# Kernel optimization log

Hardware: AMD Instinct MI355X
Metric: run time of the kernel (lower is better)

The kernel has to match this reference:

```python
import jax, jax.numpy as jnp
import numpy as np
import math

D_MODEL = 2048
N_HEADS = 16
BATCH = 2
SEQ = 2048
ALIBI_BIAS_MAX = 8


def alibi_bias(n_heads, seq_len, alibi_bias_max=8):
    # matches torch alibi_bias(full=False): shape [1, n_heads, 1, seq_len]
    dist = jnp.arange(1 - seq_len, 1, dtype=jnp.float32).reshape(1, 1, 1, seq_len)
    m = jnp.arange(1, n_heads + 1, dtype=jnp.float32) * (alibi_bias_max / n_heads)
    slopes = 1.0 / (2.0 ** m).reshape(1, n_heads, 1, 1)
    return dist * slopes


def setup_inputs() -> dict:
    key = jax.random.key(0)
    ks = jax.random.split(key, 5)
    d = D_MODEL
    scale = 1.0 / math.sqrt(d)
    x = jax.random.normal(ks[0], (BATCH, SEQ, d), dtype=jnp.float32)
    w_qkv = jax.random.normal(ks[1], (3 * d, d), dtype=jnp.float32) * scale
    b_qkv = jnp.zeros((3 * d,), dtype=jnp.float32)
    w_out = jax.random.normal(ks[2], (d, d), dtype=jnp.float32) * scale
    b_out = jnp.zeros((d,), dtype=jnp.float32)
    attn_mask = alibi_bias(N_HEADS, SEQ, ALIBI_BIAS_MAX)
    return {"x": x, "attn_mask": attn_mask, "w_qkv": w_qkv, "b_qkv": b_qkv,
            "w_out": w_out, "b_out": b_out}


def reference(x, attn_mask, w_qkv, b_qkv, w_out, b_out):
    B, S, D = x.shape
    H = N_HEADS
    hd = D // H
    # packed QKV projection
    qkv = x @ w_qkv.T + b_qkv                      # [B,S,3D]
    qkv = qkv.reshape(B, S, 3, H, hd)
    q, k, v = qkv[:, :, 0], qkv[:, :, 1], qkv[:, :, 2]  # [B,S,H,hd]
    scores = jnp.einsum('bqhd,bkhd->bhqk', q, k) * (1.0 / math.sqrt(hd))
    scores = scores + attn_mask                    # ALiBi additive bias [1,H,1,S]
    causal = jnp.tril(jnp.ones((S, S), dtype=bool))
    scores = jnp.where(causal, scores, -jnp.inf)
    probs = jax.nn.softmax(scores, axis=-1)        # [B,H,S,S]
    ctx = jnp.einsum('bhqk,bkhd->bqhd', probs, v).reshape(B, S, D)
    return ctx @ w_out.T + b_out
```

## Files before the change

### kernel.cpp

```cpp
#include <hip/hip_runtime.h>
#include <math.h>

typedef unsigned short u16;
typedef __attribute__((ext_vector_type(8))) short short8;
typedef __attribute__((ext_vector_type(4))) float f32x4;

#define MFMA16x16x32(a, b, c) __builtin_amdgcn_mfma_f32_16x16x32_bf16((a), (b), (c), 0, 0, 0)

__device__ __forceinline__ u16 f32_to_bf16(float x) {
  union { float f; unsigned u; } v; v.f = x;
  unsigned r = v.u + 0x7FFFu + ((v.u >> 16) & 1u);
  return (u16)(r >> 16);
}

__global__ void cvt_f32_bf16(const float* __restrict__ in, u16* __restrict__ out, int n4) {
  int i = blockIdx.x * blockDim.x + threadIdx.x;
  int stride = gridDim.x * blockDim.x;
  for (; i < n4; i += stride) {
    float4 v = ((const float4*)in)[i];
    ushort4 o;
    o.x = f32_to_bf16(v.x);
    o.y = f32_to_bf16(v.y);
    o.z = f32_to_bf16(v.z);
    o.w = f32_to_bf16(v.w);
    ((ushort4*)out)[i] = o;
  }
}

template <int OUT_BF16>
__global__ __launch_bounds__(256) void gemm_nt(
    const u16* __restrict__ A,
    const u16* __restrict__ B,
    const float* __restrict__ bias,
    void* __restrict__ C,
    int M, int N, int K)
{
  __shared__ u16 As[128 * 32];
  __shared__ u16 Bs[128 * 32];
  const int tid = threadIdx.x;
  const int w = tid >> 6, l = tid & 63;
  const int l15 = l & 15, l4 = l >> 4;
  const int wm = w >> 1, wn = w & 1;
  const long bm = (long)blockIdx.y * 128, bn = (long)blockIdx.x * 128;

  const f32x4 z4 = {0.f, 0.f, 0.f, 0.f};
  f32x4 acc[4][4];
  #pragma unroll
  for (int m = 0; m < 4; ++m)
    #pragma unroll
    for (int n = 0; n < 4; ++n) acc[m][n] = z4;

  const int srow = l >> 2;
  const int scol = (l & 3) * 8;

  const int nkt = K >> 5;
  for (int kt = 0; kt < nkt; ++kt) {
    const int k0 = kt << 5;
    #pragma unroll
    for (int j = 0; j < 2; ++j) {
      const int rbase = w * 32 + j * 16;
      const u16* ga = A + (bm + rbase + srow) * (long)K + k0 + scol;
      __builtin_amdgcn_global_load_lds(
          (const __attribute__((address_space(1))) void*)ga,
          (__attribute__((address_space(3))) void*)(As + rbase * 32), 16, 0, 0);
      const u16* gb = B + (bn + rbase + srow) * (long)K + k0 + scol;
      __builtin_amdgcn_global_load_lds(
          (const __attribute__((address_space(1))) void*)gb,
          (__attribute__((address_space(3))) void*)(Bs + rbase * 32), 16, 0, 0);
    }
    __syncthreads();
    short8 af[4], bf[4];
    #pragma unroll
    for (int m = 0; m < 4; ++m)
      af[m] = *(const short8*)(As + (wm * 64 + m * 16 + l15) * 32 + l4 * 8);
    #pragma unroll
    for (int n = 0; n < 4; ++n)
      bf[n] = *(const short8*)(Bs + (wn * 64 + n * 16 + l15) * 32 + l4 * 8);
    #pragma unroll
    for (int m = 0; m < 4; ++m)
      #pragma unroll
      for (int n = 0; n < 4; ++n)
        acc[m][n] = MFMA16x16x32(af[m], bf[n], acc[m][n]);
    __syncthreads();
  }

  #pragma unroll
  for (int m = 0; m < 4; ++m) {
    const long row0 = bm + wm * 64 + m * 16 + l4 * 4;
    #pragma unroll
    for (int n = 0; n < 4; ++n) {
      const long col = bn + wn * 64 + n * 16 + l15;
      const float bv = bias[col];
      #pragma unroll
      for (int r = 0; r < 4; ++r) {
        const float v = acc[m][n][r] + bv;
        if (OUT_BF16)
          ((u16*)C)[(row0 + r) * (long)N + col] = f32_to_bf16(v);
        else
          ((float*)C)[(row0 + r) * (long)N + col] = v;
      }
    }
  }
}

__global__ __launch_bounds__(256) void repack_kv(
    const u16* __restrict__ qkv, u16* __restrict__ kimg, u16* __restrict__ vimg)
{
  const int t = blockIdx.x;
  const int h = blockIdx.y, b = blockIdx.z;
  const int tid = threadIdx.x;
  __shared__ u16 Vl[64][136];

  const long qbase = ((long)(b * 2048 + t * 64)) * 6144 + h * 128;
  u16* kout = kimg + (((long)(b * 16 + h) * 32 + t) * 8192);
  u16* vout = vimg + (((long)(b * 16 + h) * 32 + t) * 8192);

  #pragma unroll
  for (int i = 0; i < 4; ++i) {
    const int j = tid + i * 256;
    {
      const int r = j >> 4, c8 = (j & 15) * 8;
      uint4 v = *(const uint4*)(qkv + qbase + (long)r * 6144 + 4096 + c8);
      *(uint4*)(&Vl[r][c8]) = v;
    }
    {
      const int byte = j * 16;
      const int r = byte >> 8;
      const int wv = (byte & 255) ^ ((r & 7) << 4);
      const int d0 = wv >> 1;
      uint4 v = *(const uint4*)(qkv + qbase + (long)r * 6144 + 2048 + d0);
      *(uint4*)(kout + j * 8) = v;
    }
  }
  __syncthreads();
  #pragma unroll
  for (int i = 0; i < 4; ++i) {
    const int j = tid + i * 256;
    const int byte = j * 16;
    const int d = byte >> 7;
    const int wv = (byte & 127) ^ ((d & 7) << 4);
    const int k0 = wv >> 1;
    u16 tmp[8];
    #pragma unroll
    for (int m = 0; m < 8; ++m) tmp[m] = Vl[k0 + m][d];
    *(uint4*)(vout + j * 8) = *(const uint4*)tmp;
  }
}

__global__ __launch_bounds__(256) void attn_kernel(
    const u16* __restrict__ qkv,
    const u16* __restrict__ kimg,
    const u16* __restrict__ vimg,
    u16* __restrict__ ctx)
{
  const int S = 2048, NHD = 6144, NT = 32;
  const int p = blockIdx.x, h = blockIdx.y, b = blockIdx.z;
  const int tid = threadIdx.x;
  const int w = tid >> 6, l = tid & 63;
  const int l15 = l & 15, l4 = l >> 4;

  __shared__ u16 Ks[64 * 128];
  __shared__ u16 Vt[128 * 64];
  __shared__ u16 Ps[4][16 * 64];

  const float LOG2E = 1.44269504088896f;
  const float c1 = 0.08838834764831845f * LOG2E;
  const float slope2 = exp2f(-0.5f * (float)(h + 1)) * LOG2E;

  const f32x4 z4 = {0.f, 0.f, 0.f, 0.f};

  for (int pass = 0; pass < 2; ++pass) {
    const int qblk = pass ? (NT - 1 - p) : p;
    const int qb0 = qblk * 64;

    short8 qf[4];
    {
      const int qrow = qb0 + w * 16 + l15;
      const u16* qp = qkv + (long)(b * S + qrow) * NHD + h * 128 + l4 * 8;
      #pragma unroll
      for (int kc = 0; kc < 4; ++kc) qf[kc] = *(const short8*)(qp + kc * 32);
    }

    f32x4 o[8];
    #pragma unroll
    for (int i = 0; i < 8; ++i) o[i] = z4;
    float m_r[4] = {-3.0e38f, -3.0e38f, -3.0e38f, -3.0e38f};
    float l_r[4] = {0.f, 0.f, 0.f, 0.f};

    for (int kt = 0; kt <= qblk; ++kt) {
      const u16* ksrc = kimg + (((long)(b * 16 + h) * NT + kt) * 8192);
      const u16* vsrc = vimg + (((long)(b * 16 + h) * NT + kt) * 8192);
      #pragma unroll
      for (int i = 0; i < 4; ++i) {
        const int chunk = w * 4 + i;
        __builtin_amdgcn_global_load_lds(
            (const __attribute__((address_space(1))) void*)(ksrc + chunk * 512 + l * 8),
            (__attribute__((address_space(3))) void*)(Ks + chunk * 512), 16, 0, 0);
        __builtin_amdgcn_global_load_lds(
            (const __attribute__((address_space(1))) void*)(vsrc + chunk * 512 + l * 8),
            (__attribute__((address_space(3))) void*)(Vt + chunk * 512), 16, 0, 0);
      }
      __syncthreads();

      f32x4 sf[4];
      #pragma unroll
      for (int nt = 0; nt < 4; ++nt) sf[nt] = z4;
      #pragma unroll
      for (int nt = 0; nt < 4; ++nt) {
        const int krow = nt * 16 + l15;
        #pragma unroll
        for (int kc = 0; kc < 4; ++kc) {
          int kbyte = (krow * 256 + kc * 64 + l4 * 16) ^ ((krow & 7) << 4);
          const short8 kf = *(const short8*)((const char*)Ks + kbyte);
          sf[nt] = MFMA16x16x32(qf[kc], kf, sf[nt]);
        }
      }

      float add_nt[4];
      int kg_nt[4];
      #pragma unroll
      for (int nt = 0; nt < 4; ++nt) {
        kg_nt[nt] = kt * 64 + nt * 16 + l15;
        add_nt[nt] = slope2 * (float)(kg_nt[nt] - (S - 1));
      }
      const bool diag = (kt == qblk);
      float alpha[4];
      #pragma unroll
      for (int r = 0; r < 4; ++r) {
        const int qrow_l = l4 * 4 + r;
        const int qg = qb0 + w * 16 + qrow_l;
        float sc[4];
        #pragma unroll
        for (int nt = 0; nt < 4; ++nt) sc[nt] = sf[nt][r] * c1 + add_nt[nt];
        if (diag) {
          #pragma unroll
          for (int nt = 0; nt < 4; ++nt)
            if (kg_nt[nt] > qg) sc[nt] = -3.0e38f;
        }
        float mx = fmaxf(fmaxf(sc[0], sc[1]), fmaxf(sc[2], sc[3]));
        #pragma unroll
        for (int d = 1; d < 16; d <<= 1) mx = fmaxf(mx, __shfl_xor(mx, d, 64));
        const float mnew = fmaxf(m_r[r], mx);
        float sum = 0.f;
        #pragma unroll
        for (int nt = 0; nt < 4; ++nt) {
          const float pv = exp2f(sc[nt] - mnew);
          sc[nt] = pv;
          sum += pv;
        }
        #pragma unroll
        for (int d = 1; d < 16; d <<= 1) sum += __shfl_xor(sum, d, 64);
        alpha[r] = exp2f(m_r[r] - mnew);
        l_r[r] = l_r[r] * alpha[r] + sum;
        m_r[r] = mnew;
        #pragma unroll
        for (int nt = 0; nt < 4; ++nt) {
          int pbyte = ((qrow_l * 64 + nt * 16 + l15) * 2) ^ ((qrow_l & 7) << 4);
          *(u16*)((char*)&Ps[w][0] + pbyte) = f32_to_bf16(sc[nt]);
        }
      }

      #pragma unroll
      for (int nt = 0; nt < 8; ++nt)
        #pragma unroll
        for (int r = 0; r < 4; ++r) o[nt][r] *= alpha[r];

      #pragma unroll
      for (int kc = 0; kc < 2; ++kc) {
        int pbyte = ((l15 * 64 + kc * 32 + l4 * 8) * 2) ^ ((l15 & 7) << 4);
        const short8 pf = *(const short8*)((const char*)&Ps[w][0] + pbyte);
        #pragma unroll
        for (int nt = 0; nt < 8; ++nt) {
          const int d = nt * 16 + l15;
          const int vbyte = ((d * 128 + kc * 64 + l4 * 16)) ^ ((d & 7) << 4);
          const short8 vf = *(const short8*)((const char*)Vt + vbyte);
          o[nt] = MFMA16x16x32(pf, vf, o[nt]);
        }
      }
      __syncthreads();
    }

    float rl[4];
    #pragma unroll
    for (int r = 0; r < 4; ++r) rl[r] = 1.0f / l_r[r];
    #pragma unroll
    for (int nt = 0; nt < 8; ++nt) {
      #pragma unroll
      for (int r = 0; r < 4; ++r) {
        const int qg = qb0 + w * 16 + l4 * 4 + r;
        ctx[(long)(b * S + qg) * 2048 + h * 128 + nt * 16 + l15] =
            f32_to_bf16(o[nt][r] * rl[r]);
      }
    }
  }
}

extern "C" void kernel_launch(void* const* d_in, const int* in_sizes, int n_in,
                              void* d_out, int out_size, void* d_ws, size_t ws_size,
                              hipStream_t stream) {
  const float* x     = (const float*)d_in[0];
  const float* w_qkv = (const float*)d_in[2];
  const float* b_qkv = (const float*)d_in[3];
  const float* w_out = (const float*)d_in[4];
  const float* b_out = (const float*)d_in[5];
  float* out = (float*)d_out;

  char* ws = (char*)d_ws;
  u16* xb    = (u16*)(ws);
  u16* wqkvb = (u16*)(ws + 16777216UL);
  u16* woutb = (u16*)(ws + 41943040UL);
  u16* qkvb  = (u16*)(ws + 50331648UL);
  u16* ctxb  = (u16*)(ws + 100663296UL);
  u16* kimg  = (u16*)(ws);
  u16* vimg  = (u16*)(ws + 16777216UL);

  cvt_f32_bf16<<<2048, 256, 0, stream>>>(x, xb, 8388608 / 4);
  cvt_f32_bf16<<<2048, 256, 0, stream>>>(w_qkv, wqkvb, 12582912 / 4);
  cvt_f32_bf16<<<2048, 256, 0, stream>>>(w_out, woutb, 4194304 / 4);

  gemm_nt<1><<<dim3(48, 32), 256, 0, stream>>>(xb, wqkvb, b_qkv, (void*)qkvb, 4096, 6144, 2048);

  repack_kv<<<dim3(32, 16, 2), 256, 0, stream>>>(qkvb, kimg, vimg);

  attn_kernel<<<dim3(16, 16, 2), 256, 0, stream>>>(qkvb, kimg, vimg, ctxb);

  gemm_nt<0><<<dim3(16, 32), 256, 0, stream>>>(ctxb, woutb, b_out, (void*)out, 4096, 2048, 2048);
}
```

Before: 352.0 us.

## Rewrite projection GEMMs with 8-wave 128x256 tiles, double-buffered swizzled LDS

Replaces the 4-wave 128x128 GEMM with an 8-wave 128x256 kernel that stages 64-wide K slices into double-buffered LDS using an XOR swizzle. The next tile's loads are issued before computing the current one, with explicit vmcnt waits. The B half-tile load is split so it overlaps the first half of the MFMA work, and s_setprio raises priority around the MFMA blocks. The aim is to hide global-load latency, avoid LDS bank conflicts and halve the barrier count per K element, at the cost of 96KB of LDS per block and hand-tuned waitcnt logic.

```diff
diff --git a/kernel.cpp b/kernel.cpp
--- a/kernel.cpp
+++ b/kernel.cpp
@@ -6,6 +6,10 @@
 typedef __attribute__((ext_vector_type(4))) float f32x4;
 
 #define MFMA16x16x32(a, b, c) __builtin_amdgcn_mfma_f32_16x16x32_bf16((a), (b), (c), 0, 0, 0)
+#define GLL16(g, s)                                                        \
+  __builtin_amdgcn_global_load_lds(                                        \
+      (const __attribute__((address_space(1))) void*)(g),                  \
+      (__attribute__((address_space(3))) void*)(s), 16, 0, 0)
 
 __device__ __forceinline__ u16 f32_to_bf16(float x) {
   union { float f; unsigned u; } v; v.f = x;
@@ -28,20 +32,36 @@
 }
 
 template <int OUT_BF16>
-__global__ __launch_bounds__(256) void gemm_nt(
+__global__ __launch_bounds__(512, 2) void gemm_nt_8p(
     const u16* __restrict__ A,
     const u16* __restrict__ B,
     const float* __restrict__ bias,
     void* __restrict__ C,
     int M, int N, int K)
 {
-  __shared__ u16 As[128 * 32];
-  __shared__ u16 Bs[128 * 32];
+  __shared__ u16 As[2][8192];
+  __shared__ u16 Bs[2][16384];
+
   const int tid = threadIdx.x;
   const int w = tid >> 6, l = tid & 63;
   const int l15 = l & 15, l4 = l >> 4;
-  const int wm = w >> 1, wn = w & 1;
-  const long bm = (long)blockIdx.y * 128, bn = (long)blockIdx.x * 128;
+  const int wm = w >> 2, wn = w & 3;
+  const long bm = (long)blockIdx.y * 128, bn = (long)blockIdx.x * 256;
+  const int NT = K >> 6;
+
+  const u16 *aSrc0, *aSrc1, *bSrc0, *bSrc1;
+  {
+    int q = w * 2048 + l * 16;
+    int r = q >> 7, cb = (q & 127) ^ ((r & 7) << 4);
+    aSrc0 = A + (bm + r) * (long)K + (cb >> 1);
+    bSrc0 = B + (bn + r) * (long)K + (cb >> 1);
+    q += 1024;
+    r = q >> 7; cb = (q & 127) ^ ((r & 7) << 4);
+    aSrc1 = A + (bm + r) * (long)K + (cb >> 1);
+    bSrc1 = B + (bn + r) * (long)K + (cb >> 1);
+  }
+  const long bHS = 128 * (long)K;
+  const int ldsA = w * 1024;
 
   const f32x4 z4 = {0.f, 0.f, 0.f, 0.f};
   f32x4 acc[4][4];
@@ -50,38 +70,81 @@
     #pragma unroll
     for (int n = 0; n < 4; ++n) acc[m][n] = z4;
 
-  const int srow = l >> 2;
-  const int scol = (l & 3) * 8;
-
-  const int nkt = K >> 5;
-  for (int kt = 0; kt < nkt; ++kt) {
-    const int k0 = kt << 5;
-    #pragma unroll
-    for (int j = 0; j < 2; ++j) {
-      const int rbase = w * 32 + j * 16;
-      const u16* ga = A + (bm + rbase + srow) * (long)K + k0 + scol;
-      __builtin_amdgcn_global_load_lds(
-          (const __attribute__((address_space(1))) void*)ga,
-          (__attribute__((address_space(3))) void*)(As + rbase * 32), 16, 0, 0);
-      const u16* gb = B + (bn + rbase + srow) * (long)K + k0 + scol;
-      __builtin_amdgcn_global_load_lds(
-          (const __attribute__((address_space(1))) void*)gb,
-          (__attribute__((address_space(3))) void*)(Bs + rbase * 32), 16, 0, 0);
-    }
-    __syncthreads();
-    short8 af[4], bf[4];
+  const int xo0 = (l4 * 16) ^ ((l15 & 7) << 4);
+  const int xo1 = (64 + l4 * 16) ^ ((l15 & 7) << 4);
+  const char* aRd = (const char*)&As[0][0] + (wm * 64 + l15) * 128;
+  const char* bRd = (const char*)&Bs[0][0] + (wn * 32 + l15) * 128;
+
+  GLL16(aSrc0, &As[0][ldsA]);
+  GLL16(aSrc1, &As[0][ldsA + 512]);
+  GLL16(bSrc0, &Bs[0][ldsA]);
+  GLL16(bSrc1, &Bs[0][ldsA + 512]);
+  GLL16(bSrc0 + bHS, &Bs[0][8192 + ldsA]);
+  GLL16(bSrc1 + bHS, &Bs[0][8192 + ldsA + 512]);
+
+  short8 af[4][2], bf[4][2];
+
+  for (int t = 0; t < NT; ++t) {
+    const int nxt = t + 1;
+    const int bufo = t & 1;
+
+    if (nxt < NT) {
+      const long ko = (long)nxt * 64;
+      const int nb = nxt & 1;
+      GLL16(aSrc0 + ko, &As[nb][ldsA]);
+      GLL16(aSrc1 + ko, &As[nb][ldsA + 512]);
+      GLL16(bSrc0 + ko, &Bs[nb][ldsA]);
+      GLL16(bSrc1 + ko, &Bs[nb][ldsA + 512]);
+      asm volatile("s_waitcnt vmcnt(6)\ns_barrier" ::: "memory");
+    } else {
+      asm volatile("s_waitcnt vmcnt(2)\ns_barrier" ::: "memory");
+    }
+    const char* ab = aRd + bufo * 16384;
+    const char* bb = bRd + bufo * 32768;
+    #pragma unroll
+    for (int m = 0; m < 4; ++m) {
+      af[m][0] = *(const short8*)(ab + m * 2048 + xo0);
+      af[m][1] = *(const short8*)(ab + m * 2048 + xo1);
+    }
+    #pragma unroll
+    for (int n = 0; n < 2; ++n) {
+      bf[n][0] = *(const short8*)(bb + n * 2048 + xo0);
+      bf[n][1] = *(const short8*)(bb + n * 2048 + xo1);
+    }
+    __builtin_amdgcn_s_setprio(1);
     #pragma unroll
     for (int m = 0; m < 4; ++m)
-      af[m] = *(const short8*)(As + (wm * 64 + m * 16 + l15) * 32 + l4 * 8);
-    #pragma unroll
-    for (int n = 0; n < 4; ++n)
-      bf[n] = *(const short8*)(Bs + (wn * 64 + n * 16 + l15) * 32 + l4 * 8);
+      #pragma unroll
+      for (int n = 0; n < 2; ++n) {
+        acc[m][n] = MFMA16x16x32(af[m][0], bf[n][0], acc[m][n]);
+        acc[m][n] = MFMA16x16x32(af[m][1], bf[n][1], acc[m][n]);
+      }
+    __builtin_amdgcn_s_setprio(0);
+
+    if (nxt < NT) {
+      const long ko = (long)nxt * 64;
+      const int nb = nxt & 1;
+      GLL16(bSrc0 + bHS + ko, &Bs[nb][8192 + ldsA]);
+      GLL16(bSrc1 + bHS + ko, &Bs[nb][8192 + ldsA + 512]);
+      asm volatile("s_waitcnt vmcnt(6)\ns_barrier" ::: "memory");
+    } else {
+      asm volatile("s_waitcnt vmcnt(0)\ns_barrier" ::: "memory");
+    }
+    const char* bb1 = bb + 16384;
+    #pragma unroll
+    for (int n = 0; n < 2; ++n) {
+      bf[2 + n][0] = *(const short8*)(bb1 + n * 2048 + xo0);
+      bf[2 + n][1] = *(const short8*)(bb1 + n * 2048 + xo1);
+    }
+    __builtin_amdgcn_s_setprio(1);
     #pragma unroll
     for (int m = 0; m < 4; ++m)
       #pragma unroll
-      for (int n = 0; n < 4; ++n)
-        acc[m][n] = MFMA16x16x32(af[m], bf[n], acc[m][n]);
-    __syncthreads();
+      for (int n = 2; n < 4; ++n) {
+        acc[m][n] = MFMA16x16x32(af[m][0], bf[n][0], acc[m][n]);
+        acc[m][n] = MFMA16x16x32(af[m][1], bf[n][1], acc[m][n]);
+      }
+    __builtin_amdgcn_s_setprio(0);
   }
 
   #pragma unroll
@@ -89,7 +152,7 @@
     const long row0 = bm + wm * 64 + m * 16 + l4 * 4;
     #pragma unroll
     for (int n = 0; n < 4; ++n) {
-      const long col = bn + wn * 64 + n * 16 + l15;
+      const long col = bn + wn * 32 + (n & 1) * 16 + (n >> 1) * 128 + l15;
       const float bv = bias[col];
       #pragma unroll
       for (int r = 0; r < 4; ++r) {
@@ -318,11 +381,11 @@
   cvt_f32_bf16<<<2048, 256, 0, stream>>>(w_qkv, wqkvb, 12582912 / 4);
   cvt_f32_bf16<<<2048, 256, 0, stream>>>(w_out, woutb, 4194304 / 4);
 
-  gemm_nt<1><<<dim3(48, 32), 256, 0, stream>>>(xb, wqkvb, b_qkv, (void*)qkvb, 4096, 6144, 2048);
+  gemm_nt_8p<1><<<dim3(24, 32), 512, 0, stream>>>(xb, wqkvb, b_qkv, (void*)qkvb, 4096, 6144, 2048);
 
   repack_kv<<<dim3(32, 16, 2), 256, 0, stream>>>(qkvb, kimg, vimg);
 
   attn_kernel<<<dim3(16, 16, 2), 256, 0, stream>>>(qkvb, kimg, vimg, ctxb);
 
-  gemm_nt<0><<<dim3(16, 32), 256, 0, stream>>>(ctxb, woutb, b_out, (void*)out, 4096, 2048, 2048);
-}
+  gemm_nt_8p<0><<<dim3(8, 32), 512, 0, stream>>>(ctxb, woutb, b_out, (void*)out, 4096, 2048, 2048);
+}
```

Result: faster. 309.9 us, median of 4 (-12.0%).

## Triple-buffer GEMM with swizzled async LDS loads and batch softmax reductions

Applied to the files above, without the earlier changes.

Rewrites the bf16 GEMM main loop as a three-stage ring of LDS buffers. Global-to-LDS loads are issued two K-tiles ahead, the layout is XOR-swizzled to avoid bank conflicts, there is one barrier per iteration, and MFMA priority is raised. It also merges the three f32-to-bf16 conversion launches into one kernel and restructures the attention softmax so the row max and sum shuffles for all four rows are interleaved. The aim is to hide global memory latency behind MFMA work, cut launch overhead and shorten shuffle dependency chains, at the cost of more LDS use (48KB per block) and tighter manual waitcnt reasoning.

```diff
diff --git a/kernel.cpp b/kernel.cpp
--- a/kernel.cpp
+++ b/kernel.cpp
@@ -6,6 +6,10 @@
 typedef __attribute__((ext_vector_type(4))) float f32x4;
 
 #define MFMA16x16x32(a, b, c) __builtin_amdgcn_mfma_f32_16x16x32_bf16((a), (b), (c), 0, 0, 0)
+#define GLL16(g, s)                                                        \
+  __builtin_amdgcn_global_load_lds(                                        \
+      (const __attribute__((address_space(1))) void*)(g),                  \
+      (__attribute__((address_space(3))) void*)(s), 16, 0, 0)
 
 __device__ __forceinline__ u16 f32_to_bf16(float x) {
   union { float f; unsigned u; } v; v.f = x;
@@ -13,35 +17,64 @@
   return (u16)(r >> 16);
 }
 
-__global__ void cvt_f32_bf16(const float* __restrict__ in, u16* __restrict__ out, int n4) {
-  int i = blockIdx.x * blockDim.x + threadIdx.x;
-  int stride = gridDim.x * blockDim.x;
-  for (; i < n4; i += stride) {
-    float4 v = ((const float4*)in)[i];
-    ushort4 o;
-    o.x = f32_to_bf16(v.x);
-    o.y = f32_to_bf16(v.y);
-    o.z = f32_to_bf16(v.z);
-    o.w = f32_to_bf16(v.w);
-    ((ushort4*)out)[i] = o;
-  }
+__device__ __forceinline__ void cvt4(const float* in, u16* out, int j) {
+  float4 v = ((const float4*)in)[j];
+  ushort4 o;
+  o.x = f32_to_bf16(v.x);
+  o.y = f32_to_bf16(v.y);
+  o.z = f32_to_bf16(v.z);
+  o.w = f32_to_bf16(v.w);
+  ((ushort4*)out)[j] = o;
+}
+
+__global__ void cvt_all(const float* __restrict__ x, const float* __restrict__ wq,
+                        const float* __restrict__ wo, u16* __restrict__ xb,
+                        u16* __restrict__ wqb, u16* __restrict__ wob) {
+  const int stride = gridDim.x * blockDim.x;
+  const int i = blockIdx.x * blockDim.x + threadIdx.x;
+  for (int j = i; j < 2097152; j += stride) cvt4(x, xb, j);
+  for (int j = i; j < 3145728; j += stride) cvt4(wq, wqb, j);
+  for (int j = i; j < 1048576; j += stride) cvt4(wo, wob, j);
 }
 
 template <int OUT_BF16>
-__global__ __launch_bounds__(256) void gemm_nt(
+__global__ __launch_bounds__(256, 3) void gemm_k32(
     const u16* __restrict__ A,
     const u16* __restrict__ B,
     const float* __restrict__ bias,
     void* __restrict__ C,
     int M, int N, int K)
 {
-  __shared__ u16 As[128 * 32];
-  __shared__ u16 Bs[128 * 32];
+  __shared__ u16 As[3][4096];
+  __shared__ u16 Bs[3][4096];
+
   const int tid = threadIdx.x;
   const int w = tid >> 6, l = tid & 63;
   const int l15 = l & 15, l4 = l >> 4;
   const int wm = w >> 1, wn = w & 1;
   const long bm = (long)blockIdx.y * 128, bn = (long)blockIdx.x * 128;
+  const int NT = K >> 5;
+
+  const int h = (l & 7) ^ (l >> 3);
+  const int rowoff = 2 * (l >> 3) + (h >> 2);
+  const int colofs = (h & 3) * 8;
+  const int c0 = (w & 1) * 4;
+  const u16* sbase = (w < 2) ? (A + bm * (long)K) : (B + bn * (long)K);
+  const u16* src0 = sbase + (long)(16 * (c0 + 0) + rowoff) * K + colofs;
+  const u16* src1 = sbase + (long)(16 * (c0 + 1) + rowoff) * K + colofs;
+  const u16* src2 = sbase + (long)(16 * (c0 + 2) + rowoff) * K + colofs;
+  const u16* src3 = sbase + (long)(16 * (c0 + 3) + rowoff) * K + colofs;
+
+#define STAGE4(tt)                                                            \
+  do {                                                                        \
+    const int _b = (tt) % 3;                                                  \
+    const long _ko = (long)(tt) * 32;                                         \
+    u16* _d = (w < 2) ? &As[_b][c0 * 512] : &Bs[_b][c0 * 512];                \
+    GLL16(src0 + _ko, _d);                                                    \
+    GLL16(src1 + _ko, _d + 512);                                              \
+    GLL16(src2 + _ko, _d + 1024);                                             \
+    GLL16(src3 + _ko, _d + 1536);                                             \
+  } while (0)
 
   const f32x4 z4 = {0.f, 0.f, 0.f, 0.f};
   f32x4 acc[4][4];
@@ -50,39 +83,40 @@
     #pragma unroll
     for (int n = 0; n < 4; ++n) acc[m][n] = z4;
 
-  const int srow = l >> 2;
-  const int scol = (l & 3) * 8;
-
-  const int nkt = K >> 5;
-  for (int kt = 0; kt < nkt; ++kt) {
-    const int k0 = kt << 5;
-    #pragma unroll
-    for (int j = 0; j < 2; ++j) {
-      const int rbase = w * 32 + j * 16;
-      const u16* ga = A + (bm + rbase + srow) * (long)K + k0 + scol;
-      __builtin_amdgcn_global_load_lds(
-          (const __attribute__((address_space(1))) void*)ga,
-          (__attribute__((address_space(3))) void*)(As + rbase * 32), 16, 0, 0);
-      const u16* gb = B + (bn + rbase + srow) * (long)K + k0 + scol;
-      __builtin_amdgcn_global_load_lds(
-          (const __attribute__((address_space(1))) void*)gb,
-          (__attribute__((address_space(3))) void*)(Bs + rbase * 32), 16, 0, 0);
-    }
-    __syncthreads();
+  const int inner = ((l15 & 1) * 64 + l4 * 16) ^ ((l15 >> 1) << 4);
+  const int rbase = (l15 >> 1) * 128 + inner;
+  const int aOfs = wm * 4096 + rbase;
+  const int bOfs = wn * 4096 + rbase;
+
+  STAGE4(0);
+  STAGE4(1);
+  asm volatile("s_waitcnt vmcnt(4)" ::: "memory");
+  __builtin_amdgcn_s_barrier();
+
+  for (int t = 0; t < NT; ++t) {
+    const char* aT = (const char*)&As[t % 3][0];
+    const char* bT = (const char*)&Bs[t % 3][0];
     short8 af[4], bf[4];
     #pragma unroll
-    for (int m = 0; m < 4; ++m)
-      af[m] = *(const short8*)(As + (wm * 64 + m * 16 + l15) * 32 + l4 * 8);
-    #pragma unroll
-    for (int n = 0; n < 4; ++n)
-      bf[n] = *(const short8*)(Bs + (wn * 64 + n * 16 + l15) * 32 + l4 * 8);
+    for (int m = 0; m < 4; ++m) af[m] = *(const short8*)(aT + aOfs + m * 1024);
+    #pragma unroll
+    for (int n = 0; n < 4; ++n) bf[n] = *(const short8*)(bT + bOfs + n * 1024);
+    if (t + 2 < NT) {
+      STAGE4(t + 2);
+      asm volatile("s_waitcnt vmcnt(4) lgkmcnt(0)" ::: "memory");
+    } else {
+      asm volatile("s_waitcnt vmcnt(0) lgkmcnt(0)" ::: "memory");
+    }
+    __builtin_amdgcn_s_setprio(1);
     #pragma unroll
     for (int m = 0; m < 4; ++m)
       #pragma unroll
       for (int n = 0; n < 4; ++n)
         acc[m][n] = MFMA16x16x32(af[m], bf[n], acc[m][n]);
-    __syncthreads();
-  }
+    __builtin_amdgcn_s_setprio(0);
+    __builtin_amdgcn_s_barrier();
+  }
+#undef STAGE4
 
   #pragma unroll
   for (int m = 0; m < 4; ++m) {
@@ -224,39 +258,53 @@
         add_nt[nt] = slope2 * (float)(kg_nt[nt] - (S - 1));
       }
       const bool diag = (kt == qblk);
-      float alpha[4];
+      float sc[4][4], mxv[4];
+      #pragma unroll
+      for (int r = 0; r < 4; ++r) {
+        const int qg = qb0 + w * 16 + l4 * 4 + r;
+        #pragma unroll
+        for (int nt = 0; nt < 4; ++nt) {
+          float s = sf[nt][r] * c1 + add_nt[nt];
+          if (diag && kg_nt[nt] > qg) s = -3.0e38f;
+          sc[r][nt] = s;
+        }
+        mxv[r] = fmaxf(fmaxf(sc[r][0], sc[r][1]), fmaxf(sc[r][2], sc[r][3]));
+      }
+      #pragma unroll
+      for (int d = 1; d < 16; d <<= 1) {
+        #pragma unroll
+        for (int r = 0; r < 4; ++r)
+          mxv[r] = fmaxf(mxv[r], __shfl_xor(mxv[r], d, 64));
+      }
+      float alpha[4], sum[4];
+      #pragma unroll
+      for (int r = 0; r < 4; ++r) {
+        const float mnew = fmaxf(m_r[r], mxv[r]);
+        sum[r] = 0.f;
+        #pragma unroll
+        for (int nt = 0; nt < 4; ++nt) {
+          const float pv = exp2f(sc[r][nt] - mnew);
+          sc[r][nt] = pv;
+          sum[r] += pv;
+        }
+        alpha[r] = exp2f(m_r[r] - mnew);
+        m_r[r] = mnew;
+      }
+      #pragma unroll
+      for (int d = 1; d < 16; d <<= 1) {
+        #pragma unroll
+        for (int r = 0; r < 4; ++r) sum[r] += __shfl_xor(sum[r], d, 64);
+      }
+      #pragma unroll
+      for (int r = 0; r < 4; ++r) l_r[r] = l_r[r] * alpha[r] + sum[r];
+
       #pragma unroll
       for (int r = 0; r < 4; ++r) {
         const int qrow_l = l4 * 4 + r;
-        const int qg = qb0 + w * 16 + qrow_l;
-        float sc[4];
-        #pragma unroll
-        for (int nt = 0; nt < 4; ++nt) sc[nt] = sf[nt][r] * c1 + add_nt[nt];
-        if (diag) {
-          #pragma unroll
-          for (int nt = 0; nt < 4; ++nt)
-            if (kg_nt[nt] > qg) sc[nt] = -3.0e38f;
-        }
-        float mx = fmaxf(fmaxf(sc[0], sc[1]), fmaxf(sc[2], sc[3]));
-        #pragma unroll
-        for (int d = 1; d < 16; d <<= 1) mx = fmaxf(mx, __shfl_xor(mx, d, 64));
-        const float mnew = fmaxf(m_r[r], mx);
-        float sum = 0.f;
-        #pragma unroll
-        for (int nt = 0; nt < 4; ++nt) {
-          const float pv = exp2f(sc[nt] - mnew);
-          sc[nt] = pv;
-          sum += pv;
-        }
-        #pragma unroll
-        for (int d = 1; d < 16; d <<= 1) sum += __shfl_xor(sum, d, 64);
-        alpha[r] = exp2f(m_r[r] - mnew);
-        l_r[r] = l_r[r] * alpha[r] + sum;
-        m_r[r] = mnew;
         #pragma unroll
         for (int nt = 0; nt < 4; ++nt) {
           int pbyte = ((qrow_l * 64 + nt * 16 + l15) * 2) ^ ((qrow_l & 7) << 4);
-          *(u16*)((char*)&Ps[w][0] + pbyte) = f32_to_bf16(sc[nt]);
+          *(u16*)((char*)&Ps[w][0] + pbyte) = f32_to_bf16(sc[r][nt]);
         }
       }
 
@@ -314,15 +362,13 @@
   u16* kimg  = (u16*)(ws);
   u16* vimg  = (u16*)(ws + 16777216UL);
 
-  cvt_f32_bf16<<<2048, 256, 0, stream>>>(x, xb, 8388608 / 4);
-  cvt_f32_bf16<<<2048, 256, 0, stream>>>(w_qkv, wqkvb, 12582912 / 4);
-  cvt_f32_bf16<<<2048, 256, 0, stream>>>(w_out, woutb, 4194304 / 4);
-
-  gemm_nt<1><<<dim3(48, 32), 256, 0, stream>>>(xb, wqkvb, b_qkv, (void*)qkvb, 4096, 6144, 2048);
+  cvt_all<<<2048, 256, 0, stream>>>(x, w_qkv, w_out, xb, wqkvb, woutb);
+
+  gemm_k32<1><<<dim3(48, 32), 256, 0, stream>>>(xb, wqkvb, b_qkv, (void*)qkvb, 4096, 6144, 2048);
 
   repack_kv<<<dim3(32, 16, 2), 256, 0, stream>>>(qkvb, kimg, vimg);
 
   attn_kernel<<<dim3(16, 16, 2), 256, 0, stream>>>(qkvb, kimg, vimg, ctxb);
 
-  gemm_nt<0><<<dim3(16, 32), 256, 0, stream>>>(ctxb, woutb, b_out, (void*)out, 4096, 2048, 2048);
-}
+  gemm_k32<0><<<dim3(16, 32), 256, 0, stream>>>(ctxb, woutb, b_out, (void*)out, 4096, 2048, 2048);
+}
```

Result: faster. 303.3 us (-13.8%).
